# Optimization experiments

Hardware: AMD Instinct MI355X
Metric: run time of the kernel (lower is better)

Reference implementation:

```python
import jax
import jax.numpy as jnp
import numpy as np

T, B = 128, 64
A_DIM, Z_DIM, K_MIX = 32, 64, 16
HIDDEN, NUM_LAYERS = 128, 2
Q_REG = 1e-3
R_REG = 1e-3


def _lstm_layer(x, Wih, Whh, bih, bhh):
    # x: [T, B, in]; torch gate order i, f, g, o
    H = Whh.shape[1]
    h0 = jnp.zeros((x.shape[1], H), x.dtype)

    def step(carry, xt):
        h, c = carry
        gates = xt @ Wih.T + bih + h @ Whh.T + bhh
        i, f, g, o = jnp.split(gates, 4, axis=-1)
        c = jax.nn.sigmoid(f) * c + jax.nn.sigmoid(i) * jnp.tanh(g)
        h = jax.nn.sigmoid(o) * jnp.tanh(c)
        return (h, c), h

    _, hs = jax.lax.scan(step, (h0, h0), x)
    return hs


def _weights(as_, lstm_params, lin_W, lin_b):
    x = as_
    for (Wih, Whh, bih, bhh) in lstm_params:
        x = _lstm_layer(x, Wih, Whh, bih, bhh)
    logits = x @ lin_W.T + lin_b  # [T, B, K]
    return jax.nn.softmax(logits, axis=-1)


def setup_inputs() -> dict:
    key = jax.random.key(0)
    ks = jax.random.split(key, 16)
    inp = {
        "as_": jax.random.normal(ks[0], (T, B, A_DIM), jnp.float32),
        # 0.3 scale keeps the mixture transition matrix spectral radius < 1
        "mat_A_K": 0.3 * jax.random.normal(ks[1], (K_MIX, Z_DIM, Z_DIM), jnp.float32),
        "mat_C_K": jax.random.normal(ks[2], (K_MIX, A_DIM, Z_DIM), jnp.float32),
        "Q_L": jax.random.normal(ks[3], (Z_DIM, Z_DIM), jnp.float32),
        "R_L": jax.random.normal(ks[4], (A_DIM, A_DIM), jnp.float32),
        "lin_W": jax.random.normal(ks[5], (K_MIX, HIDDEN), jnp.float32) / np.sqrt(HIDDEN),
        "lin_b": jnp.zeros((K_MIX,), jnp.float32),
    }
    s = 1.0 / np.sqrt(HIDDEN)
    for l in range(NUM_LAYERS):
        in_dim = A_DIM if l == 0 else HIDDEN
        k1, k2 = jax.random.split(jax.random.fold_in(key, 100 + l))
        inp[f"lstm_Wih{l}"] = s * jax.random.normal(k1, (4 * HIDDEN, in_dim), jnp.float32)
        inp[f"lstm_Whh{l}"] = s * jax.random.normal(k2, (4 * HIDDEN, HIDDEN), jnp.float32)
        inp[f"lstm_bih{l}"] = jnp.zeros((4 * HIDDEN,), jnp.float32)
        inp[f"lstm_bhh{l}"] = jnp.zeros((4 * HIDDEN,), jnp.float32)
    return inp


def reference(as_, mat_A_K, mat_C_K, Q_L, R_L, lin_W, lin_b,
              lstm_Wih0, lstm_Whh0, lstm_bih0, lstm_bhh0,
              lstm_Wih1, lstm_Whh1, lstm_bih1, lstm_bhh1):
    lstm_params = [(lstm_Wih0, lstm_Whh0, lstm_bih0, lstm_bhh0),
                   (lstm_Wih1, lstm_Whh1, lstm_bih1, lstm_bhh1)]
    w = _weights(as_, lstm_params, lin_W, lin_b)            # [T, B, K]
    mat_As = jnp.einsum('tbk,kij->tbij', w, mat_A_K)         # [T, B, z, z]
    mat_Cs = jnp.einsum('tbk,kij->tbij', w, mat_C_K)         # [T, B, a, z]

    I_z = jnp.eye(Z_DIM, dtype=as_.dtype)
    I_a = jnp.eye(A_DIM, dtype=as_.dtype)
    Q = Q_L @ Q_L.T + Q_REG * I_z
    R = R_L @ R_L.T + R_REG * I_a

    mean0 = jnp.zeros((B, Z_DIM, 1), as_.dtype)              # initial_state_mean = 0
    cov0 = jnp.broadcast_to(I_z, (B, Z_DIM, Z_DIM))          # initial_state_covariance = I

    def sym(M):
        return 0.5 * (M + jnp.swapaxes(M, 1, 2))

    def step(carry, inp):
        mean_p, cov_p = carry
        A_t, C_t, a_t = inp                                   # [B,z,z], [B,a,z], [B,a]
        C_tT = jnp.swapaxes(C_t, 1, 2)
        S = C_t @ cov_p @ C_tT + R                            # [B, a, a]
        K_t = cov_p @ C_tT @ jnp.linalg.inv(S)                # [B, z, a]
        mean_t = mean_p + K_t @ (a_t[..., None] - C_t @ mean_p)
        mean_next = A_t @ mean_t
        cov_t = sym(cov_p - K_t @ C_t @ cov_p)
        cov_next = sym(A_t @ cov_t @ jnp.swapaxes(A_t, 1, 2) + Q)
        return (mean_next, cov_next), (mean_t, cov_t, mean_next, cov_next)

    _, (means, covs, next_means, next_covs) = jax.lax.scan(
        step, (mean0, cov0), (mat_As, mat_Cs, as_))
    return means, covs, next_means, next_covs, mat_As, mat_Cs
```

## Files before the change

### kernel.cpp

```cpp
#include <hip/hip_runtime.h>
#include <math.h>

#define T_LEN 128
#define B_SZ  64
#define AD    32
#define ZD    64
#define KMIX  16
#define HID   128

#define WS_B0 106496
#define WS_B1 107008
#define WS_Q  107520
#define WS_R  111616
#define WS_W  112640

#define OUT_MEANS   0
#define OUT_COVS    524288
#define OUT_NMEANS  34078720
#define OUT_NCOVS   34603008
#define OUT_MATA    68157440
#define OUT_MATC    101711872

__device__ __forceinline__ float sigmoidf_(float x){ return 1.0f/(1.0f + expf(-x)); }

__device__ __forceinline__ unsigned short f2bf(float f){
  unsigned u = __float_as_uint(f);
  u += 0x7FFFu + ((u >> 16) & 1u);
  return (unsigned short)(u >> 16);
}

__global__ __launch_bounds__(256) void prep_kernel(
    const float* __restrict__ Wih0, const float* __restrict__ Whh0,
    const float* __restrict__ bih0, const float* __restrict__ bhh0,
    const float* __restrict__ Wih1, const float* __restrict__ Whh1,
    const float* __restrict__ bih1, const float* __restrict__ bhh1,
    const float* __restrict__ QL,   const float* __restrict__ RL,
    float* __restrict__ ws)
{
  int idx = blockIdx.x*256 + threadIdx.x;
  unsigned short* w16 = (unsigned short*)ws;
  if (idx < 212992) {
    const float* src; int local, base, IN;
    if (idx < 16384)       { src = Wih0; local = idx;          base = 0;      IN = 32; }
    else if (idx < 81920)  { src = Whh0; local = idx - 16384;  base = 16384;  IN = 128; }
    else if (idx < 147456) { src = Wih1; local = idx - 81920;  base = 81920;  IN = 128; }
    else                   { src = Whh1; local = idx - 147456; base = 147456; IN = 128; }
    int pair = local >> 10, g = (local >> 1) & 511, lo = local & 1;
    int k = pair*2 + lo;
    w16[base + local] = f2bf(src[g*IN + k]);
  } else if (idx < 213504) {
    int g = idx - 212992; ws[WS_B0 + g] = bih0[g] + bhh0[g];
  } else if (idx < 214016) {
    int g = idx - 213504; ws[WS_B1 + g] = bih1[g] + bhh1[g];
  } else if (idx < 218112) {
    int e = idx - 214016; int i = e >> 6, j = e & 63;
    float s = (i==j) ? 1e-3f : 0.f;
    for (int k = 0; k < 64; ++k) s += QL[i*64+k]*QL[j*64+k];
    ws[WS_Q + e] = s;
  } else if (idx < 219136) {
    int e = idx - 218112; int i = e >> 5, j = e & 31;
    float s = (i==j) ? 1e-3f : 0.f;
    for (int k = 0; k < 32; ++k) s += RL[i*32+k]*RL[j*32+k];
    ws[WS_R + e] = s;
  }
}

__global__ __launch_bounds__(512) void lstm_kernel(
    const float* __restrict__ as_, const float* __restrict__ ws,
    const float* __restrict__ linW, const float* __restrict__ linb,
    float* __restrict__ wout)
{
  const int b = blockIdx.x, tid = threadIdx.x;
  const unsigned* W0ih = (const unsigned*)ws;
  const unsigned* W0hh = W0ih + 16*512;
  const unsigned* W1ih = W0hh + 64*512;
  const unsigned* W1hh = W1ih + 64*512;

  __shared__ float xs[2][32];
  __shared__ float h0[128];
  __shared__ float h1[128];
  __shared__ float gbuf[512];
  __shared__ float lw[16*132];

  for (int e = tid; e < 2048; e += 512) lw[(e >> 7)*132 + (e & 127)] = linW[e];
  if (tid < 128) { h0[tid] = 0.f; h1[tid] = 0.f; }
  if (tid < 32)  xs[0][tid] = as_[(0*B_SZ + b)*AD + tid];
  float c0 = 0.f, c1 = 0.f;
  const float bias0 = ws[WS_B0 + tid];
  const float bias1 = ws[WS_B1 + tid];
  const float lbk = linb[tid & 15];
  __syncthreads();

  for (int t = 0; t < T_LEN; ++t) {
    const int cp = t & 1, np = cp ^ 1;
    {
      float acc = bias0;
      #pragma unroll 4
      for (int kk = 0; kk < 16; ++kk) {
        const unsigned u = W0ih[kk*512 + tid];
        acc += __uint_as_float(u << 16) * xs[cp][2*kk]
             + __uint_as_float(u & 0xFFFF0000u) * xs[cp][2*kk+1];
      }
      #pragma unroll 8
      for (int kk = 0; kk < 64; ++kk) {
        const unsigned u = W0hh[kk*512 + tid];
        acc += __uint_as_float(u << 16) * h0[2*kk]
             + __uint_as_float(u & 0xFFFF0000u) * h0[2*kk+1];
      }
      gbuf[tid] = acc;
    }
    __syncthreads();
    if (tid < 128) {
      float ig = sigmoidf_(gbuf[tid]);
      float fg = sigmoidf_(gbuf[tid+128]);
      float gg = tanhf(gbuf[tid+256]);
      float og = sigmoidf_(gbuf[tid+384]);
      c0 = fg*c0 + ig*gg;
      h0[tid] = og * tanhf(c0);
    } else if (tid < 160 && t+1 < T_LEN) {
      xs[np][tid-128] = as_[((t+1)*B_SZ + b)*AD + (tid-128)];
    }
    __syncthreads();
    {
      float acc = bias1;
      #pragma unroll 8
      for (int kk = 0; kk < 64; ++kk) {
        const unsigned u = W1ih[kk*512 + tid];
        acc += __uint_as_float(u << 16) * h0[2*kk]
             + __uint_as_float(u & 0xFFFF0000u) * h0[2*kk+1];
      }
      #pragma unroll 8
      for (int kk = 0; kk < 64; ++kk) {
        const unsigned u = W1hh[kk*512 + tid];
        acc += __uint_as_float(u << 16) * h1[2*kk]
             + __uint_as_float(u & 0xFFFF0000u) * h1[2*kk+1];
      }
      gbuf[tid] = acc;
    }
    __syncthreads();
    if (tid < 128) {
      float ig = sigmoidf_(gbuf[tid]);
      float fg = sigmoidf_(gbuf[tid+128]);
      float gg = tanhf(gbuf[tid+256]);
      float og = sigmoidf_(gbuf[tid+384]);
      c1 = fg*c1 + ig*gg;
      h1[tid] = og * tanhf(c1);
    }
    __syncthreads();
    if (tid < 64) {
      const int k = tid & 15, q = tid >> 4;
      float acc = 0.f;
      const float* lr = &lw[k*132 + q*32];
      const float* hr = &h1[q*32];
      #pragma unroll 8
      for (int j = 0; j < 32; ++j) acc += lr[j] * hr[j];
      acc += __shfl_xor(acc, 16);
      acc += __shfl_xor(acc, 32);
      const float logit = acc + lbk;
      float m = logit;
      m = fmaxf(m, __shfl_xor(m, 1));
      m = fmaxf(m, __shfl_xor(m, 2));
      m = fmaxf(m, __shfl_xor(m, 4));
      m = fmaxf(m, __shfl_xor(m, 8));
      const float e = expf(logit - m);
      float s = e;
      s += __shfl_xor(s, 1); s += __shfl_xor(s, 2);
      s += __shfl_xor(s, 4); s += __shfl_xor(s, 8);
      if (tid < 16) wout[(t*B_SZ + b)*KMIX + k] = e / s;
    }
  }
}

__global__ __launch_bounds__(256) void mix_kernel(
    const float* __restrict__ w, const float* __restrict__ AK,
    const float* __restrict__ CK, float* __restrict__ out)
{
  float* matA = out + OUT_MATA;
  float* matC = out + OUT_MATC;
  const int tb0 = blockIdx.x * 16;
  const int tid = threadIdx.x;
  __shared__ float wl[16][16];
  { int lt = tid >> 4, k = tid & 15; wl[lt][k] = w[(tb0 + lt)*16 + k]; }
  __syncthreads();

  for (int e = tid; e < ZD*ZD; e += 256) {
    float v[16];
    #pragma unroll
    for (int u = 0; u < 16; ++u) v[u] = 0.f;
    #pragma unroll 4
    for (int k = 0; k < 16; ++k) {
      float a = AK[k*ZD*ZD + e];
      #pragma unroll
      for (int u = 0; u < 16; ++u) v[u] += wl[u][k] * a;
    }
    #pragma unroll
    for (int u = 0; u < 16; ++u) matA[(size_t)(tb0+u)*(ZD*ZD) + e] = v[u];
  }
  for (int e = tid; e < AD*ZD; e += 256) {
    float v[16];
    #pragma unroll
    for (int u = 0; u < 16; ++u) v[u] = 0.f;
    #pragma unroll 4
    for (int k = 0; k < 16; ++k) {
      float a = CK[k*AD*ZD + e];
      #pragma unroll
      for (int u = 0; u < 16; ++u) v[u] += wl[u][k] * a;
    }
    #pragma unroll
    for (int u = 0; u < 16; ++u) matC[(size_t)(tb0+u)*(AD*ZD) + e] = v[u];
  }
}

__global__ __launch_bounds__(512, 1) void kalman_kernel(
    const float* __restrict__ as_, const float* __restrict__ ws,
    float* __restrict__ out)
{
  const int b = blockIdx.x, tid = threadIdx.x;
  const float* Rm = ws + WS_R;
  const float* Qg = ws + WS_Q;
  const float* matA = out + OUT_MATA;
  const float* matC = out + OUT_MATC;
  float* means  = out + OUT_MEANS;
  float* covs   = out + OUT_COVS;
  float* nmeans = out + OUT_NMEANS;
  float* ncovs  = out + OUT_NCOVS;

  __shared__ __align__(16) float covp[64*68];
  __shared__ __align__(16) float At[2][64*68];
  __shared__ __align__(16) float Cm[2][32*68];
  __shared__ __align__(16) float CPm[32*68];
  __shared__ __align__(16) float Wm[32*68];
  __shared__ float Smat[32*36];
  __shared__ __align__(16) float tmpm[64*68];
  __shared__ __align__(16) float Ql[64*68];

  for (int e = tid; e < 64*64; e += 512) {
    const int i = e >> 6, j = e & 63;
    Ql[i*68 + j]   = Qg[e];
    covp[i*68 + j] = (i == j) ? 1.f : 0.f;
  }
  if (tid < 64) covp[tid*68 + 64] = 0.f;
  {
    const float* Ag = matA + (size_t)b*4096;
    const float* Cg = matC + (size_t)b*2048;
    for (int e = tid; e < 4096; e += 512) At[0][(e & 63)*68 + (e >> 6)] = Ag[e];
    for (int e = tid; e < 2048; e += 512) Cm[0][(e >> 6)*68 + (e & 63)] = Cg[e];
  }
  __syncthreads();

  const int su = tid - 128;

  int cur = 0;
  for (int t = 0; t < T_LEN; ++t) {
    const int tb = t*B_SZ + b;
    const int nxt = cur ^ 1;
    float areg = 0.f;
    if ((tid & 15) == 15) areg = as_[(size_t)tb*AD + (tid >> 4)];

    {
      const int i = tid >> 4, j0 = (tid & 15)*4;
      const bool do64 = ((tid & 15) == 15);
      const float* Crow = &Cm[cur][i*68];
      float4 acc = make_float4(0,0,0,0); float s64 = 0.f;
      #pragma unroll 4
      for (int k4 = 0; k4 < 16; ++k4) {
        const float4 a4 = *(const float4*)&Crow[k4*4];
        const float4 b0 = *(const float4*)&covp[(k4*4+0)*68 + j0];
        const float4 b1 = *(const float4*)&covp[(k4*4+1)*68 + j0];
        const float4 b2 = *(const float4*)&covp[(k4*4+2)*68 + j0];
        const float4 b3 = *(const float4*)&covp[(k4*4+3)*68 + j0];
        acc.x += a4.x*b0.x + a4.y*b1.x + a4.z*b2.x + a4.w*b3.x;
        acc.y += a4.x*b0.y + a4.y*b1.y + a4.z*b2.y + a4.w*b3.y;
        acc.z += a4.x*b0.z + a4.y*b1.z + a4.z*b2.z + a4.w*b3.z;
        acc.w += a4.x*b0.w + a4.y*b1.w + a4.z*b2.w + a4.w*b3.w;
        if (do64) {
          s64 += a4.x*covp[(k4*4+0)*68+64] + a4.y*covp[(k4*4+1)*68+64]
               + a4.z*covp[(k4*4+2)*68+64] + a4.w*covp[(k4*4+3)*68+64];
        }
      }
      *(float4*)&CPm[i*68 + j0] = acc;
      if (do64) CPm[i*68 + 64] = s64 - areg;
    }
    __syncthreads();
    {
      const int i = tid >> 4, j0 = (tid & 15)*2;
      const float* CProw = &CPm[i*68];
      const float* Cr0 = &Cm[cur][(j0+0)*68];
      const float* Cr1 = &Cm[cur][(j0+1)*68];
      float a0 = 0.f, a1 = 0.f;
      #pragma unroll 4
      for (int k4 = 0; k4 < 16; ++k4) {
        const float4 cp4 = *(const float4*)&CProw[k4*4];
        const float4 c04 = *(const float4*)&Cr0[k4*4];
        const float4 c14 = *(const float4*)&Cr1[k4*4];
        a0 += cp4.x*c04.x + cp4.y*c04.y + cp4.z*c04.z + cp4.w*c04.w;
        a1 += cp4.x*c14.x + cp4.y*c14.y + cp4.z*c14.z + cp4.w*c14.w;
      }
      Smat[i*36 + j0+0] = a0 + Rm[i*32 + j0+0];
      Smat[i*36 + j0+1] = a1 + Rm[i*32 + j0+1];
    }
    __syncthreads();
    {
      const int wv = tid >> 6, lane = tid & 63;
      if (wv == 0) {
        if (lane < 32) {
          float Lr[32];
          float invd = 0.f;
          #pragma unroll
          for (int j = 0; j < 32; ++j) Lr[j] = Smat[lane*36 + j];
          #pragma unroll
          for (int k = 0; k < 32; ++k) {
            const float piv = __shfl(Lr[k], k);
            const float ir  = 1.0f / sqrtf(piv);
            const float lik = Lr[k] * ir;
            invd = (lane == k) ? ir : invd;
            #pragma unroll
            for (int j = k+1; j < 32; ++j) {
              const float ljk = __shfl(lik, j);
              Lr[j] -= lik * ljk;
            }
            Lr[k] = lik;
          }
          #pragma unroll
          for (int j = 0; j < 32; ++j)
            if (j < lane) Smat[lane*36 + j] = Lr[j];
          Smat[lane*36 + lane] = invd;
        }
      } else if (wv >= 2 && t < T_LEN-1) {
        const float* Ag = matA + (size_t)(tb+64)*4096;
        const float* Cg = matC + (size_t)(tb+64)*2048;
        const float4 q0 = *(const float4*)&Ag[su*4];
        const float4 q1 = *(const float4*)&Ag[(su+384)*4];
        const float4 q2 = (su < 256) ? *(const float4*)&Ag[(su+768)*4]
                                     : *(const float4*)&Cg[(su-256)*4];
        const float4 q3 = *(const float4*)&Cg[(su+128)*4];
        { const int c = su;       const int i = c>>4, j = (c&15)*4;
          At[nxt][(j+0)*68+i]=q0.x; At[nxt][(j+1)*68+i]=q0.y; At[nxt][(j+2)*68+i]=q0.z; At[nxt][(j+3)*68+i]=q0.w; }
        { const int c = su + 384; const int i = c>>4, j = (c&15)*4;
          At[nxt][(j+0)*68+i]=q1.x; At[nxt][(j+1)*68+i]=q1.y; At[nxt][(j+2)*68+i]=q1.z; At[nxt][(j+3)*68+i]=q1.w; }
        if (su < 256) { const int c = su + 768; const int i = c>>4, j = (c&15)*4;
          At[nxt][(j+0)*68+i]=q2.x; At[nxt][(j+1)*68+i]=q2.y; At[nxt][(j+2)*68+i]=q2.z; At[nxt][(j+3)*68+i]=q2.w; }
        else { const int cc = su - 256; *(float4*)&Cm[nxt][(cc>>4)*68 + (cc&15)*4] = q2; }
        { const int cc = su + 128;      *(float4*)&Cm[nxt][(cc>>4)*68 + (cc&15)*4] = q3; }
      }
    }
    __syncthreads();
    if (tid < 65) {
      const int c = tid;
      float s[32];
      #pragma unroll
      for (int i = 0; i < 32; ++i) s[i] = CPm[i*68 + c];
      #pragma unroll
      for (int k = 0; k < 32; ++k) {
        const float y = s[k] * Smat[k*36 + k];
        Wm[k*68 + c] = y;
        #pragma unroll
        for (int i = k+1; i < 32; ++i)
          s[i] -= Smat[i*36 + k] * y;
      }
    }
    __syncthreads();
    {
      const int j = tid >> 3, c0 = (tid & 7)*8;
      const bool do64 = ((tid & 7) == 7);
      float4 a0 = make_float4(0,0,0,0), a1 = a0; float s64 = 0.f;
      #pragma unroll 8
      for (int k = 0; k < 32; ++k) {
        const float a = Wm[k*68 + j];
        const float4 b0 = *(const float4*)&Wm[k*68 + c0];
        const float4 b1 = *(const float4*)&Wm[k*68 + c0 + 4];
        a0.x += a*b0.x; a0.y += a*b0.y; a0.z += a*b0.z; a0.w += a*b0.w;
        a1.x += a*b1.x; a1.y += a*b1.y; a1.z += a*b1.z; a1.w += a*b1.w;
        if (do64) s64 += a * Wm[k*68 + 64];
      }
      float4 c4a = *(const float4*)&covp[j*68 + c0];
      float4 c4b = *(const float4*)&covp[j*68 + c0 + 4];
      c4a.x -= a0.x; c4a.y -= a0.y; c4a.z -= a0.z; c4a.w -= a0.w;
      c4b.x -= a1.x; c4b.y -= a1.y; c4b.z -= a1.z; c4b.w -= a1.w;
      *(float4*)&covp[j*68 + c0]     = c4a;
      *(float4*)&covp[j*68 + c0 + 4] = c4b;
      *(float4*)&covs[(size_t)tb*4096 + j*64 + c0]     = c4a;
      *(float4*)&covs[(size_t)tb*4096 + j*64 + c0 + 4] = c4b;
      if (do64) {
        const float mt = covp[j*68 + 64] - s64;
        covp[j*68 + 64] = mt;
        means[(size_t)tb*64 + j] = mt;
      }
    }
    __syncthreads();
    {
      const int i = tid >> 3, c0 = (tid & 7)*8;
      const bool do64 = ((tid & 7) == 7);
      const float* Atb = At[cur];
      float4 a0 = make_float4(0,0,0,0), a1 = a0; float s64 = 0.f;
      #pragma unroll 8
      for (int k = 0; k < 64; ++k) {
        const float a = Atb[k*68 + i];
        const float4 b0 = *(const float4*)&covp[k*68 + c0];
        const float4 b1 = *(const float4*)&covp[k*68 + c0 + 4];
        a0.x += a*b0.x; a0.y += a*b0.y; a0.z += a*b0.z; a0.w += a*b0.w;
        a1.x += a*b1.x; a1.y += a*b1.y; a1.z += a*b1.z; a1.w += a*b1.w;
        if (do64) s64 += a * covp[k*68 + 64];
      }
      *(float4*)&tmpm[i*68 + c0]     = a0;
      *(float4*)&tmpm[i*68 + c0 + 4] = a1;
      if (do64) {
        tmpm[i*68 + 64] = s64;
        nmeans[(size_t)tb*64 + i] = s64;
      }
    }
    __syncthreads();
    {
      const int i = tid >> 3, j0 = (tid & 7)*8;
      const float* Atb  = At[cur];
      const float* trow = &tmpm[i*68];
      float4 a0 = make_float4(0,0,0,0), a1 = a0;
      #pragma unroll 4
      for (int k4 = 0; k4 < 16; ++k4) {
        const float4 t4 = *(const float4*)&trow[k4*4];
        #pragma unroll
        for (int m = 0; m < 4; ++m) {
          const float a = (m==0)?t4.x:(m==1)?t4.y:(m==2)?t4.z:t4.w;
          const float4 b0 = *(const float4*)&Atb[(k4*4+m)*68 + j0];
          const float4 b1 = *(const float4*)&Atb[(k4*4+m)*68 + j0 + 4];
          a0.x += a*b0.x; a0.y += a*b0.y; a0.z += a*b0.z; a0.w += a*b0.w;
          a1.x += a*b1.x; a1.y += a*b1.y; a1.z += a*b1.z; a1.w += a*b1.w;
        }
      }
      const float4 q0 = *(const float4*)&Ql[i*68 + j0];
      const float4 q1 = *(const float4*)&Ql[i*68 + j0 + 4];
      a0.x += q0.x; a0.y += q0.y; a0.z += q0.z; a0.w += q0.w;
      a1.x += q1.x; a1.y += q1.y; a1.z += q1.z; a1.w += q1.w;
      *(float4*)&covp[i*68 + j0]     = a0;
      *(float4*)&covp[i*68 + j0 + 4] = a1;
      *(float4*)&ncovs[(size_t)tb*4096 + i*64 + j0]     = a0;
      *(float4*)&ncovs[(size_t)tb*4096 + i*64 + j0 + 4] = a1;
      if ((tid & 7) == 7) covp[i*68 + 64] = tmpm[i*68 + 64];
    }
    __syncthreads();
    cur = nxt;
  }
}

extern "C" void kernel_launch(void* const* d_in, const int* in_sizes, int n_in,
                              void* d_out, int out_size, void* d_ws, size_t ws_size,
                              hipStream_t stream) {
  const float* as_  = (const float*)d_in[0];
  const float* AK   = (const float*)d_in[1];
  const float* CK   = (const float*)d_in[2];
  const float* QL   = (const float*)d_in[3];
  const float* RL   = (const float*)d_in[4];
  const float* linW = (const float*)d_in[5];
  const float* linb = (const float*)d_in[6];
  const float* Wih0 = (const float*)d_in[7];
  const float* Whh0 = (const float*)d_in[8];
  const float* bih0 = (const float*)d_in[9];
  const float* bhh0 = (const float*)d_in[10];
  const float* Wih1 = (const float*)d_in[11];
  const float* Whh1 = (const float*)d_in[12];
  const float* bih1 = (const float*)d_in[13];
  const float* bhh1 = (const float*)d_in[14];
  float* out = (float*)d_out;
  float* ws  = (float*)d_ws;

  prep_kernel<<<856, 256, 0, stream>>>(Wih0, Whh0, bih0, bhh0,
                                       Wih1, Whh1, bih1, bhh1, QL, RL, ws);
  lstm_kernel<<<B_SZ, 512, 0, stream>>>(as_, ws, linW, linb, ws + WS_W);
  mix_kernel<<<(T_LEN*B_SZ)/16, 256, 0, stream>>>(ws + WS_W, AK, CK, out);
  kalman_kernel<<<B_SZ, 512, 0, stream>>>(as_, ws, out);
}
```

Before: 4.219 ms.

## Restructure Kalman covariance update to overlap A·P product with Cholesky

The predicted covariance is now computed as A·P·Aᵀ + Q − (A·Wᵀ)(A·Wᵀ)ᵀ. This lets the A·P_prior product (U) run on idle warps in parallel with the Cholesky factorization, instead of waiting for the corrected covariance. Removing the dependency on the updated covariance drops one barrier-separated stage from the serial per-timestep chain. The prefetch of the next A/C moves into the triangular-solve phase, and a small V = W·Aᵀ product is added. The cost is extra FLOPs (the U product covers 65 columns plus the V correction) and different floating-point rounding from the algebraic reordering.

```diff
diff --git a/kernel.cpp b/kernel.cpp
--- a/kernel.cpp
+++ b/kernel.cpp
@@ -211,6 +211,21 @@
   }
 }
 
+__device__ __forceinline__ void u_slot(const float* __restrict__ Atc,
+                                       const float* __restrict__ cov,
+                                       float* __restrict__ Um, int ii, int qq)
+{
+  const int c0 = qq*4;
+  float4 acc = make_float4(0,0,0,0);
+  #pragma unroll 8
+  for (int k = 0; k < 64; ++k) {
+    const float a = Atc[k*68 + ii];
+    const float4 b4 = *(const float4*)&cov[k*68 + c0];
+    acc.x += a*b4.x; acc.y += a*b4.y; acc.z += a*b4.z; acc.w += a*b4.w;
+  }
+  *(float4*)&Um[ii*68 + c0] = acc;
+}
+
 __global__ __launch_bounds__(512, 1) void kalman_kernel(
     const float* __restrict__ as_, const float* __restrict__ ws,
     float* __restrict__ out)
@@ -231,15 +246,17 @@
   __shared__ __align__(16) float CPm[32*68];
   __shared__ __align__(16) float Wm[32*68];
   __shared__ float Smat[32*36];
-  __shared__ __align__(16) float tmpm[64*68];
+  __shared__ __align__(16) float Um[64*68];
+  __shared__ __align__(16) float Vt[32*68];
   __shared__ __align__(16) float Ql[64*68];
 
+  for (int e = tid; e < 64*68; e += 512) covp[e] = 0.f;
+  __syncthreads();
   for (int e = tid; e < 64*64; e += 512) {
     const int i = e >> 6, j = e & 63;
     Ql[i*68 + j]   = Qg[e];
     covp[i*68 + j] = (i == j) ? 1.f : 0.f;
   }
-  if (tid < 64) covp[tid*68 + 64] = 0.f;
   {
     const float* Ag = matA + (size_t)b*4096;
     const float* Cg = matC + (size_t)b*2048;
@@ -247,8 +264,6 @@
     for (int e = tid; e < 2048; e += 512) Cm[0][(e >> 6)*68 + (e & 63)] = Cg[e];
   }
   __syncthreads();
-
-  const int su = tid - 128;
 
   int cur = 0;
   for (int t = 0; t < T_LEN; ++t) {
@@ -326,7 +341,31 @@
             if (j < lane) Smat[lane*36 + j] = Lr[j];
           Smat[lane*36 + lane] = invd;
         }
-      } else if (wv >= 2 && t < T_LEN-1) {
+      } else {
+        const int su2 = tid - 64;
+        const float* Atc = At[cur];
+        { const int s = su2;       u_slot(Atc, covp, Um, s & 63, s >> 6); }
+        { const int s = su2 + 448; u_slot(Atc, covp, Um, s & 63, s >> 6); }
+        if (su2 < 192) { const int s = su2 + 896; u_slot(Atc, covp, Um, s & 63, s >> 6); }
+      }
+    }
+    __syncthreads();
+    {
+      if (tid < 65) {
+        const int c = tid;
+        float s[32];
+        #pragma unroll
+        for (int i = 0; i < 32; ++i) s[i] = CPm[i*68 + c];
+        #pragma unroll
+        for (int k = 0; k < 32; ++k) {
+          const float y = s[k] * Smat[k*36 + k];
+          Wm[k*68 + c] = y;
+          #pragma unroll
+          for (int i = k+1; i < 32; ++i)
+            s[i] -= Smat[i*36 + k] * y;
+        }
+      } else if (tid >= 128 && t < T_LEN-1) {
+        const int su = tid - 128;
         const float* Ag = matA + (size_t)(tb+64)*4096;
         const float* Cg = matC + (size_t)(tb+64)*2048;
         const float4 q0 = *(const float4*)&Ag[su*4];
@@ -345,21 +384,6 @@
       }
     }
     __syncthreads();
-    if (tid < 65) {
-      const int c = tid;
-      float s[32];
-      #pragma unroll
-      for (int i = 0; i < 32; ++i) s[i] = CPm[i*68 + c];
-      #pragma unroll
-      for (int k = 0; k < 32; ++k) {
-        const float y = s[k] * Smat[k*36 + k];
-        Wm[k*68 + c] = y;
-        #pragma unroll
-        for (int i = k+1; i < 32; ++i)
-          s[i] -= Smat[i*36 + k] * y;
-      }
-    }
-    __syncthreads();
     {
       const int j = tid >> 3, c0 = (tid & 7)*8;
       const bool do64 = ((tid & 7) == 7);
@@ -377,65 +401,67 @@
       float4 c4b = *(const float4*)&covp[j*68 + c0 + 4];
       c4a.x -= a0.x; c4a.y -= a0.y; c4a.z -= a0.z; c4a.w -= a0.w;
       c4b.x -= a1.x; c4b.y -= a1.y; c4b.z -= a1.z; c4b.w -= a1.w;
-      *(float4*)&covp[j*68 + c0]     = c4a;
-      *(float4*)&covp[j*68 + c0 + 4] = c4b;
       *(float4*)&covs[(size_t)tb*4096 + j*64 + c0]     = c4a;
       *(float4*)&covs[(size_t)tb*4096 + j*64 + c0 + 4] = c4b;
-      if (do64) {
-        const float mt = covp[j*68 + 64] - s64;
-        covp[j*68 + 64] = mt;
-        means[(size_t)tb*64 + j] = mt;
-      }
-    }
-    __syncthreads();
-    {
-      const int i = tid >> 3, c0 = (tid & 7)*8;
-      const bool do64 = ((tid & 7) == 7);
-      const float* Atb = At[cur];
-      float4 a0 = make_float4(0,0,0,0), a1 = a0; float s64 = 0.f;
-      #pragma unroll 8
-      for (int k = 0; k < 64; ++k) {
-        const float a = Atb[k*68 + i];
-        const float4 b0 = *(const float4*)&covp[k*68 + c0];
-        const float4 b1 = *(const float4*)&covp[k*68 + c0 + 4];
-        a0.x += a*b0.x; a0.y += a*b0.y; a0.z += a*b0.z; a0.w += a*b0.w;
-        a1.x += a*b1.x; a1.y += a*b1.y; a1.z += a*b1.z; a1.w += a*b1.w;
-        if (do64) s64 += a * covp[k*68 + 64];
-      }
-      *(float4*)&tmpm[i*68 + c0]     = a0;
-      *(float4*)&tmpm[i*68 + c0 + 4] = a1;
-      if (do64) {
-        tmpm[i*68 + 64] = s64;
-        nmeans[(size_t)tb*64 + i] = s64;
-      }
+      if (do64) means[(size_t)tb*64 + j] = covp[j*68 + 64] - s64;
+    }
+    {
+      const int a = tid & 31, c0 = (tid >> 5)*4;
+      const float* Wr  = &Wm[a*68];
+      const float* Atc = At[cur];
+      float4 acc = make_float4(0,0,0,0);
+      #pragma unroll 4
+      for (int k4 = 0; k4 < 16; ++k4) {
+        const float4 w4 = *(const float4*)&Wr[k4*4];
+        const float4 b0 = *(const float4*)&Atc[(k4*4+0)*68 + c0];
+        const float4 b1 = *(const float4*)&Atc[(k4*4+1)*68 + c0];
+        const float4 b2 = *(const float4*)&Atc[(k4*4+2)*68 + c0];
+        const float4 b3 = *(const float4*)&Atc[(k4*4+3)*68 + c0];
+        acc.x += w4.x*b0.x + w4.y*b1.x + w4.z*b2.x + w4.w*b3.x;
+        acc.y += w4.x*b0.y + w4.y*b1.y + w4.z*b2.y + w4.w*b3.y;
+        acc.z += w4.x*b0.z + w4.y*b1.z + w4.z*b2.z + w4.w*b3.z;
+        acc.w += w4.x*b0.w + w4.y*b1.w + w4.z*b2.w + w4.w*b3.w;
+      }
+      *(float4*)&Vt[a*68 + c0] = acc;
     }
     __syncthreads();
     {
       const int i = tid >> 3, j0 = (tid & 7)*8;
-      const float* Atb  = At[cur];
-      const float* trow = &tmpm[i*68];
-      float4 a0 = make_float4(0,0,0,0), a1 = a0;
+      const float* Atc  = At[cur];
+      const float* trow = &Um[i*68];
+      float4 a0 = *(const float4*)&Ql[i*68 + j0];
+      float4 a1 = *(const float4*)&Ql[i*68 + j0 + 4];
       #pragma unroll 4
       for (int k4 = 0; k4 < 16; ++k4) {
         const float4 t4 = *(const float4*)&trow[k4*4];
         #pragma unroll
         for (int m = 0; m < 4; ++m) {
           const float a = (m==0)?t4.x:(m==1)?t4.y:(m==2)?t4.z:t4.w;
-          const float4 b0 = *(const float4*)&Atb[(k4*4+m)*68 + j0];
-          const float4 b1 = *(const float4*)&Atb[(k4*4+m)*68 + j0 + 4];
+          const float4 b0 = *(const float4*)&Atc[(k4*4+m)*68 + j0];
+          const float4 b1 = *(const float4*)&Atc[(k4*4+m)*68 + j0 + 4];
           a0.x += a*b0.x; a0.y += a*b0.y; a0.z += a*b0.z; a0.w += a*b0.w;
           a1.x += a*b1.x; a1.y += a*b1.y; a1.z += a*b1.z; a1.w += a*b1.w;
         }
       }
-      const float4 q0 = *(const float4*)&Ql[i*68 + j0];
-      const float4 q1 = *(const float4*)&Ql[i*68 + j0 + 4];
-      a0.x += q0.x; a0.y += q0.y; a0.z += q0.z; a0.w += q0.w;
-      a1.x += q1.x; a1.y += q1.y; a1.z += q1.z; a1.w += q1.w;
+      #pragma unroll 8
+      for (int a = 0; a < 32; ++a) {
+        const float va = Vt[a*68 + i];
+        const float4 b0 = *(const float4*)&Vt[a*68 + j0];
+        const float4 b1 = *(const float4*)&Vt[a*68 + j0 + 4];
+        a0.x -= va*b0.x; a0.y -= va*b0.y; a0.z -= va*b0.z; a0.w -= va*b0.w;
+        a1.x -= va*b1.x; a1.y -= va*b1.y; a1.z -= va*b1.z; a1.w -= va*b1.w;
+      }
       *(float4*)&covp[i*68 + j0]     = a0;
       *(float4*)&covp[i*68 + j0 + 4] = a1;
       *(float4*)&ncovs[(size_t)tb*4096 + i*64 + j0]     = a0;
       *(float4*)&ncovs[(size_t)tb*4096 + i*64 + j0 + 4] = a1;
-      if ((tid & 7) == 7) covp[i*68 + 64] = tmpm[i*68 + 64];
+      if ((tid & 7) == 7) {
+        float s64 = Um[i*68 + 64];
+        #pragma unroll 8
+        for (int a = 0; a < 32; ++a) s64 -= Vt[a*68 + i] * Wm[a*68 + 64];
+        covp[i*68 + 64] = s64;
+        nmeans[(size_t)tb*64 + i] = s64;
+      }
     }
     __syncthreads();
     cur = nxt;
```

Result: no change. 4.145 ms (-1.8%).
